# Optimization experiments

Hardware: AMD Instinct MI355X
Metric: run time of the kernel (lower is better)

The kernel has to match this reference:

```python
import jax, jax.numpy as jnp
import numpy as np

N_NODES = 4194304  # 2**22
LEVELS = 10
COARSE = 8192
RANK = 2
NNZ = 8388608


def _interp_linear(u, N):
    """torch F.interpolate(mode='linear', align_corners=False) along axis 1. u: (B,M,R) -> (B,N,R)."""
    M = u.shape[1]
    pos = (jnp.arange(N, dtype=jnp.float32) + 0.5) * (M / N) - 0.5
    pos = jnp.clip(pos, 0.0, M - 1)
    i0 = jnp.floor(pos).astype(jnp.int32)
    i1 = jnp.minimum(i0 + 1, M - 1)
    w = (pos - i0.astype(jnp.float32))[None, :, None]
    return u[:, i0] * (1.0 - w) + u[:, i1] * w


def _apply_hodlr(diag, u_factors, v_factors, x):
    B, N, _ = x.shape
    y = diag * x
    L = u_factors.shape[0]
    for lvl in range(L):
        num_splits = 2 ** (lvl + 1)
        bs = N // num_splits
        if bs == 0:
            continue
        uc, vc = u_factors[lvl], v_factors[lvl]
        u_full = _interp_linear(uc, N) if uc.shape[1] != N else uc
        v_full = _interp_linear(vc, N) if vc.shape[1] != N else vc
        P = num_splits // 2
        valid = P * 2 * bs
        xv = x[:, :valid].reshape(B, P, 2, bs, 1)
        uv = u_full[:, :valid].reshape(B, P, 2, bs, -1)
        vv = v_full[:, :valid].reshape(B, P, 2, bs, -1)
        xL, xR = xv[:, :, 0], xv[:, :, 1]
        uL, uR = uv[:, :, 0], uv[:, :, 1]
        vL, vR = vv[:, :, 0], vv[:, :, 1]
        xRp = jnp.einsum('bpkr,bpko->bpro', vR, xR)  # (B,P,R,1)
        xLp = jnp.einsum('bpkr,bpko->bpro', vL, xL)
        yL = jnp.einsum('bpkr,bpro->bpko', uL, xRp)  # (B,P,bs,1)
        yR = jnp.einsum('bpkr,bpro->bpko', uR, xLp)
        upd = jnp.stack([yL, yR], axis=2).reshape(B, valid, 1)
        if valid < N:
            upd = jnp.pad(upd, ((0, 0), (0, N - valid), (0, 0)))
        y = y + upd
    return y


def setup_inputs() -> dict:
    key = jax.random.key(0)
    ks = jax.random.split(key, 6)
    diag = jax.random.uniform(ks[0], (1, N_NODES, 1), dtype=jnp.float32)
    u_factors = jax.random.normal(ks[1], (LEVELS, 1, COARSE, RANK), dtype=jnp.float32)
    v_factors = jax.random.normal(ks[2], (LEVELS, 1, COARSE, RANK), dtype=jnp.float32)
    A_values = jax.random.normal(ks[3], (NNZ,), dtype=jnp.float32)
    z = jax.random.normal(ks[4], (1, N_NODES, 1), dtype=jnp.float32)
    A_indices = jax.random.randint(ks[5], (2, NNZ), 0, N_NODES, dtype=jnp.int64) if jax.config.jax_enable_x64 else jax.random.randint(ks[5], (2, NNZ), 0, N_NODES, dtype=jnp.int32)
    return {"diag": diag, "u_factors": u_factors, "v_factors": v_factors,
            "A_values": A_values, "z": z, "A_indices": A_indices, "num_nodes": N_NODES}


def reference(diag, u_factors, v_factors, A_values, z, A_indices, num_nodes):
    N = num_nodes
    w = _apply_hodlr(diag, u_factors, v_factors, z)          # (1,N,1)
    w_flat = w.reshape(N)
    rows, cols = A_indices[0], A_indices[1]
    y_flat = jax.ops.segment_sum(A_values * w_flat[cols], rows, num_segments=N)
    y = y_flat.reshape(1, N, 1)
    loss = jnp.mean((y - z) ** 2)
    return loss
```

## Files before the change

kernel.cpp:

```cpp
#include <hip/hip_runtime.h>

#define N_NODES 4194304
#define LEVELS  10
#define COARSE  8192
#define NNZ_E   8388608
#define NSEG    512
#define RB_SZ   8192
#define EPB     8192
#define CAP_SEG 18432u

typedef int          v4i __attribute__((ext_vector_type(4)));
typedef float        v4f __attribute__((ext_vector_type(4)));
typedef unsigned int v4u __attribute__((ext_vector_type(4)));

static __device__ __forceinline__ unsigned short f2bf(float x) {
    unsigned u = __float_as_uint(x);
    return (unsigned short)((u + 0x7FFFu + ((u >> 16) & 1u)) >> 16);
}
static __device__ __forceinline__ float bf2f(unsigned short h) {
    return __uint_as_float((unsigned)h << 16);
}

__global__ __launch_bounds__(512) void k1(const float* __restrict__ z,
                                          float2* __restrict__ M,
                                          float* __restrict__ S,
                                          float* __restrict__ out) {
    int b = blockIdx.x, t = threadIdx.x;
    if (b == 0) {
        for (int i = t; i < 2046 * 2; i += 512) S[i] = 0.f;
        if (t == 0) out[0] = 0.f;
    }
    int lane = t & 63, wave = t >> 6;
    int chunk = b * 8 + wave;
    int base = chunk * 256 + lane * 4;
    float4 zv = *(const float4*)(z + base);
    float a0 = 0.f, a1 = 0.f;
    const float* zp = (const float*)&zv;
#pragma unroll
    for (int j = 0; j < 4; ++j) {
        float p = ((float)(base + j) + 0.5f) * (1.0f / 512.0f) - 0.5f;
        p = fminf(fmaxf(p, 0.0f), (float)(COARSE - 1));
        float f = p - floorf(p);
        a0 += zp[j] * (1.0f - f);
        a1 += zp[j] * f;
    }
#pragma unroll
    for (int off = 32; off >= 1; off >>= 1) {
        a0 += __shfl_xor(a0, off, 64);
        a1 += __shfl_xor(a1, off, 64);
    }
    if (lane == 0) M[chunk] = make_float2(a0, a1);
}

__global__ __launch_bounds__(256) void kB(const float2* __restrict__ M,
                                          const float* __restrict__ V,
                                          float* __restrict__ S) {
    int b = blockIdx.x, t = threadIdx.x;
    int lvl = b >> 3, slice = b & 7;
    const float2* Vl = (const float2*)(V + lvl * COARSE * 2);
    float s0 = 0.f, s1 = 0.f;
    int c0 = slice * 2048 + t * 8;
#pragma unroll
    for (int cc = 0; cc < 8; ++cc) {
        int c = c0 + cc;
        float2 m = M[c];
        int k = (c > 0) ? ((c - 1) >> 1) : 0;
        int kp = min(k + 1, COARSE - 1);
        float2 vk = Vl[k], vkp = Vl[kp];
        s0 += vk.x * m.x + vkp.x * m.y;
        s1 += vk.y * m.x + vkp.y * m.y;
    }
    int gw = min(1 << (10 - lvl), 64);
    for (int sh = gw >> 1; sh >= 1; sh >>= 1) {
        s0 += __shfl_xor(s0, sh, 64);
        s1 += __shfl_xor(s1, sh, 64);
    }
    if ((t & (gw - 1)) == 0) {
        int bb = c0 >> (13 - lvl);
        int soff = (2 << lvl) - 2;
        unsafeAtomicAdd(&S[(soff + bb) * 2 + 0], s0);
        unsafeAtomicAdd(&S[(soff + bb) * 2 + 1], s1);
    }
}

__global__ __launch_bounds__(512) void kCw(const float* __restrict__ diag,
                                           const float* __restrict__ z,
                                           const float* __restrict__ S,
                                           const float* __restrict__ U,
                                           unsigned short* __restrict__ wb) {
    int b = blockIdx.x, t = threadIdx.x;
    int tid = b * 512 + t;
    int base = tid * 4;
    int c = base >> 8;
    int k = (c > 0) ? ((c - 1) >> 1) : 0;
    int kp = min(k + 1, COARSE - 1);
    float g0 = 0.f, g1 = 0.f;
#pragma unroll
    for (int lvl = 0; lvl < LEVELS; ++lvl) {
        int sib = (c >> (13 - lvl)) ^ 1;
        int soff = (2 << lvl) - 2;
        float2 s2 = ((const float2*)S)[soff + sib];
        const float2* Ul = (const float2*)(U + lvl * COARSE * 2);
        float2 uk = Ul[k], ukp = Ul[kp];
        g0 += uk.x * s2.x + uk.y * s2.y;
        g1 += ukp.x * s2.x + ukp.y * s2.y;
    }
    float4 d4 = *(const float4*)(diag + base);
    float4 z4 = *(const float4*)(z + base);
    const float* dp = (const float*)&d4;
    const float* zp = (const float*)&z4;
    ushort4 h4;
    unsigned short* hp = (unsigned short*)&h4;
#pragma unroll
    for (int j = 0; j < 4; ++j) {
        float p = ((float)(base + j) + 0.5f) * (1.0f / 512.0f) - 0.5f;
        p = fminf(fmaxf(p, 0.0f), (float)(COARSE - 1));
        float f = p - floorf(p);
        hp[j] = f2bf(dp[j] * zp[j] + (g0 + f * (g1 - g0)));
    }
    *(ushort4*)(wb + base) = h4;
}

__global__ __launch_bounds__(1024) void k2(const int* __restrict__ rows,
                                           const int* __restrict__ cols,
                                           const float* __restrict__ vals,
                                           const unsigned short* __restrict__ wb,
                                           unsigned* __restrict__ segCtr,
                                           unsigned* __restrict__ binned) {
    __shared__ unsigned sortedP[EPB];
    __shared__ unsigned short sortedB[EPB];
    __shared__ unsigned cur[NSEG], gb[NSEG];
    __shared__ unsigned wsum[16], wbase[16];
    int blk = blockIdx.x, t = threadIdx.x;
    int base = blk * EPB;
    v4i r[2], c[2];
    v4f v[2];
#pragma unroll
    for (int j = 0; j < 2; ++j) {
        int e = base + j * 4096 + t * 4;
        r[j] = __builtin_nontemporal_load((const v4i*)(rows + e));
        c[j] = __builtin_nontemporal_load((const v4i*)(cols + e));
        v[j] = __builtin_nontemporal_load((const v4f*)(vals + e));
    }
    float wf[8];
#pragma unroll 1
    for (int p = 0; p < 4; ++p) {
#pragma unroll
        for (int j = 0; j < 2; ++j) {
            const int* cp = (const int*)&c[j];
#pragma unroll
            for (int kk = 0; kk < 4; ++kk) {
                unsigned cc = (unsigned)cp[kk];
                if ((cc >> 20) == (unsigned)p)
                    wf[j * 4 + kk] = bf2f(wb[cc]);
            }
        }
        __syncthreads();
    }
    if (t < NSEG) cur[t] = 0u;
    __syncthreads();
#pragma unroll
    for (int j = 0; j < 2; ++j) {
        const int* rp = (const int*)&r[j];
#pragma unroll
        for (int kk = 0; kk < 4; ++kk)
            atomicAdd(&cur[(unsigned)rp[kk] >> 13], 1u);
    }
    __syncthreads();
    unsigned lv = 0, lincl = 0;
    if (t < NSEG) {
        lv = cur[t];
        lincl = lv;
#pragma unroll
        for (int off = 1; off < 64; off <<= 1) {
            unsigned n = __shfl_up(lincl, off, 64);
            if ((t & 63) >= off) lincl += n;
        }
        if ((t & 63) == 63) wsum[t >> 6] = lincl;
    }
    __syncthreads();
    if (t == 0) {
        unsigned a = 0;
        for (int i = 0; i < 8; ++i) { wbase[i] = a; a += wsum[i]; }
    }
    __syncthreads();
    if (t < NSEG) {
        unsigned lexcl = wbase[t >> 6] + lincl - lv;
        gb[t] = (unsigned)t * CAP_SEG + atomicAdd(&segCtr[t], lv) - lexcl;
        cur[t] = lexcl;
    }
    __syncthreads();
#pragma unroll
    for (int j = 0; j < 2; ++j) {
        const int* rp = (const int*)&r[j];
        const float* vp = (const float*)&v[j];
#pragma unroll
        for (int kk = 0; kk < 4; ++kk) {
            unsigned row = (unsigned)rp[kk];
            unsigned seg = row >> 13;
            unsigned rl = row & 8191u;
            float p = wf[j * 4 + kk] * vp[kk];
            unsigned pe = ((__float_as_uint(p) + 0x1000u) >> 13) & 0x7FFFFu;
            unsigned i = atomicAdd(&cur[seg], 1u);
            sortedP[i] = (rl << 19) | pe;
            sortedB[i] = (unsigned short)seg;
        }
    }
    __syncthreads();
#pragma unroll
    for (int k = 0; k < 8; ++k) {
        int i = k * 1024 + t;
        unsigned s = sortedB[i];
        __builtin_nontemporal_store(sortedP[i], binned + gb[s] + i);
    }
}

__global__ __launch_bounds__(1024) void kE(const unsigned* __restrict__ binned,
                                           const unsigned* __restrict__ segCtr,
                                           const float* __restrict__ z,
                                           float* __restrict__ out) {
    __shared__ float acc[RB_SZ];
    __shared__ float red[16];
    int b = blockIdx.x, t = threadIdx.x;

    for (int i = t; i < RB_SZ / 4; i += 1024) ((float4*)acc)[i] = make_float4(0.f, 0.f, 0.f, 0.f);
    __syncthreads();

    unsigned n = segCtr[b];
    const unsigned* seg = binned + (size_t)b * CAP_SEG;
    unsigned i = t;
    for (; i + 7u * 1024u < n; i += 8u * 1024u) {
        unsigned ev[8];
#pragma unroll
        for (int k = 0; k < 8; ++k)
            ev[k] = __builtin_nontemporal_load(seg + i + (unsigned)k * 1024u);
#pragma unroll
        for (int k = 0; k < 8; ++k)
            atomicAdd(&acc[ev[k] >> 19], __uint_as_float((ev[k] & 0x7FFFFu) << 13));
    }
    for (; i < n; i += 1024u) {
        unsigned e = __builtin_nontemporal_load(seg + i);
        atomicAdd(&acc[e >> 19], __uint_as_float((e & 0x7FFFFu) << 13));
    }
    __syncthreads();

    float part = 0.f;
    int gbase = b * RB_SZ;
    for (int k = t; k < RB_SZ; k += 1024) {
        float d = acc[k] - z[gbase + k];
        part += d * d;
    }
#pragma unroll
    for (int off = 32; off >= 1; off >>= 1) part += __shfl_xor(part, off, 64);
    if ((t & 63) == 0) red[t >> 6] = part;
    __syncthreads();
    if (t == 0) {
        float s = 0.f;
        for (int k = 0; k < 16; ++k) s += red[k];
        unsafeAtomicAdd(out, s * (1.0f / (float)N_NODES));
    }
}

extern "C" void kernel_launch(void* const* d_in, const int* in_sizes, int n_in,
                              void* d_out, int out_size, void* d_ws, size_t ws_size,
                              hipStream_t stream) {
    const float* diag  = (const float*)d_in[0];
    const float* U     = (const float*)d_in[1];
    const float* V     = (const float*)d_in[2];
    const float* Avals = (const float*)d_in[3];
    const float* z     = (const float*)d_in[4];
    const int*   Aidx  = (const int*)d_in[5];
    const int* rows = Aidx;
    const int* cols = Aidx + NNZ_E;

    char* ws = (char*)d_ws;
    size_t off = 0;
    unsigned short* wb  = (unsigned short*)(ws + off); off += (size_t)N_NODES * 2;
    unsigned* binned    = (unsigned*)(ws + off);       off += (size_t)NSEG * CAP_SEG * 4;
    unsigned* segCtr    = (unsigned*)(ws + off);       off += NSEG * 4;
    float2* M           = (float2*)(ws + off);         off += (size_t)(N_NODES / 256) * 8;
    float* S            = (float*)(ws + off);          off += 16384;

    hipMemsetAsync(segCtr, 0, NSEG * 4, stream);
    k1<<<2048, 512, 0, stream>>>(z, M, S, (float*)d_out);
    kB<<<80, 256, 0, stream>>>(M, V, S);
    kCw<<<2048, 512, 0, stream>>>(diag, z, S, U, wb);
    k2<<<1024, 1024, 0, stream>>>(rows, cols, Avals, wb, segCtr, binned);
    kE<<<NSEG, 1024, 0, stream>>>(binned, segCtr, z, (float*)d_out);
}
```

Before: 302.6 us.

## Split gather and row-binning into separate kernels, fold counter reset into k1

```diff
diff --git a/kernel.cpp b/kernel.cpp
--- a/kernel.cpp
+++ b/kernel.cpp
@@ -24,11 +24,13 @@
 __global__ __launch_bounds__(512) void k1(const float* __restrict__ z,
                                           float2* __restrict__ M,
                                           float* __restrict__ S,
-                                          float* __restrict__ out) {
+                                          float* __restrict__ out,
+                                          unsigned* __restrict__ segCtr) {
     int b = blockIdx.x, t = threadIdx.x;
     if (b == 0) {
         for (int i = t; i < 2046 * 2; i += 512) S[i] = 0.f;
         if (t == 0) out[0] = 0.f;
+        segCtr[t] = 0u;
     }
     int lane = t & 63, wave = t >> 6;
     int chunk = b * 8 + wave;
@@ -121,24 +123,17 @@
     *(ushort4*)(wb + base) = h4;
 }
 
-__global__ __launch_bounds__(1024) void k2(const int* __restrict__ rows,
-                                           const int* __restrict__ cols,
-                                           const float* __restrict__ vals,
-                                           const unsigned short* __restrict__ wb,
-                                           unsigned* __restrict__ segCtr,
-                                           unsigned* __restrict__ binned) {
-    __shared__ unsigned sortedP[EPB];
-    __shared__ unsigned short sortedB[EPB];
-    __shared__ unsigned cur[NSEG], gb[NSEG];
-    __shared__ unsigned wsum[16], wbase[16];
-    int blk = blockIdx.x, t = threadIdx.x;
-    int base = blk * EPB;
-    v4i r[2], c[2];
+__global__ __launch_bounds__(512) void kG(const int* __restrict__ cols,
+                                          const float* __restrict__ vals,
+                                          const unsigned short* __restrict__ wb,
+                                          float* __restrict__ wp) {
+    int b = blockIdx.x, t = threadIdx.x;
+    int base = b * 4096;
+    v4i c[2];
     v4f v[2];
 #pragma unroll
     for (int j = 0; j < 2; ++j) {
-        int e = base + j * 4096 + t * 4;
-        r[j] = __builtin_nontemporal_load((const v4i*)(rows + e));
+        int e = base + j * 2048 + t * 4;
         c[j] = __builtin_nontemporal_load((const v4i*)(cols + e));
         v[j] = __builtin_nontemporal_load((const v4f*)(vals + e));
     }
@@ -157,6 +152,36 @@
         }
         __syncthreads();
     }
+#pragma unroll
+    for (int j = 0; j < 2; ++j) {
+        const float* vp = (const float*)&v[j];
+        v4f o;
+        float* op = (float*)&o;
+#pragma unroll
+        for (int kk = 0; kk < 4; ++kk) op[kk] = wf[j * 4 + kk] * vp[kk];
+        int e = base + j * 2048 + t * 4;
+        __builtin_nontemporal_store(o, (v4f*)(wp + e));
+    }
+}
+
+__global__ __launch_bounds__(1024) void k2s(const int* __restrict__ rows,
+                                            const float* __restrict__ wp,
+                                            unsigned* __restrict__ segCtr,
+                                            unsigned* __restrict__ binned) {
+    __shared__ unsigned sortedP[EPB];
+    __shared__ unsigned short sortedB[EPB];
+    __shared__ unsigned cur[NSEG], gb[NSEG];
+    __shared__ unsigned wsum[16], wbase[16];
+    int blk = blockIdx.x, t = threadIdx.x;
+    int base = blk * EPB;
+    v4i r[2];
+    v4f p4[2];
+#pragma unroll
+    for (int j = 0; j < 2; ++j) {
+        int e = base + j * 4096 + t * 4;
+        r[j] = __builtin_nontemporal_load((const v4i*)(rows + e));
+        p4[j] = __builtin_nontemporal_load((const v4f*)(wp + e));
+    }
     if (t < NSEG) cur[t] = 0u;
     __syncthreads();
 #pragma unroll
@@ -193,14 +218,13 @@
 #pragma unroll
     for (int j = 0; j < 2; ++j) {
         const int* rp = (const int*)&r[j];
-        const float* vp = (const float*)&v[j];
+        const float* pp = (const float*)&p4[j];
 #pragma unroll
         for (int kk = 0; kk < 4; ++kk) {
             unsigned row = (unsigned)rp[kk];
             unsigned seg = row >> 13;
             unsigned rl = row & 8191u;
-            float p = wf[j * 4 + kk] * vp[kk];
-            unsigned pe = ((__float_as_uint(p) + 0x1000u) >> 13) & 0x7FFFFu;
+            unsigned pe = ((__float_as_uint(pp[kk]) + 0x1000u) >> 13) & 0x7FFFFu;
             unsigned i = atomicAdd(&cur[seg], 1u);
             sortedP[i] = (rl << 19) | pe;
             sortedB[i] = (unsigned short)seg;
@@ -277,14 +301,15 @@
     size_t off = 0;
     unsigned short* wb  = (unsigned short*)(ws + off); off += (size_t)N_NODES * 2;
     unsigned* binned    = (unsigned*)(ws + off);       off += (size_t)NSEG * CAP_SEG * 4;
+    float* wp           = (float*)(ws + off);          off += (size_t)NNZ_E * 4;
     unsigned* segCtr    = (unsigned*)(ws + off);       off += NSEG * 4;
     float2* M           = (float2*)(ws + off);         off += (size_t)(N_NODES / 256) * 8;
     float* S            = (float*)(ws + off);          off += 16384;
 
-    hipMemsetAsync(segCtr, 0, NSEG * 4, stream);
-    k1<<<2048, 512, 0, stream>>>(z, M, S, (float*)d_out);
+    k1<<<2048, 512, 0, stream>>>(z, M, S, (float*)d_out, segCtr);
     kB<<<80, 256, 0, stream>>>(M, V, S);
     kCw<<<2048, 512, 0, stream>>>(diag, z, S, U, wb);
-    k2<<<1024, 1024, 0, stream>>>(rows, cols, Avals, wb, segCtr, binned);
+    kG<<<2048, 512, 0, stream>>>(cols, Avals, wb, wp);
+    k2s<<<1024, 1024, 0, stream>>>(rows, wp, segCtr, binned);
     kE<<<NSEG, 1024, 0, stream>>>(binned, segCtr, z, (float*)d_out);
 }
```

Measured after the change: 304.2 us. No clear change (+0.5%).
